# Kernel tuning notes

Measured on AMD Instinct MI355X. Metric: run time of the kernel, lower is better.

## Reference

```python
import jax, jax.numpy as jnp
import numpy as np

N_NODES = 50000
N_EDGES = 800000
C_IN = 128
HID = 128
C_OUT = 128


def _glorot(key, shape):
    fan_in, fan_out = shape
    lim = (6.0 / (fan_in + fan_out)) ** 0.5
    return jax.random.uniform(key, shape, jnp.float32, -lim, lim)


def setup_inputs() -> dict:
    key = jax.random.key(0)
    ks = jax.random.split(key, 8)
    x = jax.random.normal(ks[0], (N_NODES, C_IN), jnp.float32)
    edge_index = jax.random.randint(ks[1], (2, N_EDGES), 0, N_NODES, jnp.int32)
    return {
        "x": x,
        "edge_index": edge_index,
        # nn_in: Lin(2*C_IN, HID) -> ReLU -> Lin(HID, HID)
        "W1_in": _glorot(ks[2], (2 * C_IN, HID)), "b1_in": jnp.zeros((HID,), jnp.float32),
        "W2_in": _glorot(ks[3], (HID, HID)), "b2_in": jnp.zeros((HID,), jnp.float32),
        # nn_hid: Lin(2*HID, HID) -> ReLU -> Lin(HID, HID)
        "W1_hid": _glorot(ks[4], (2 * HID, HID)), "b1_hid": jnp.zeros((HID,), jnp.float32),
        "W2_hid": _glorot(ks[5], (HID, HID)), "b2_hid": jnp.zeros((HID,), jnp.float32),
        # nn_out: Lin(2*HID, HID) -> ReLU -> Lin(HID, C_OUT)
        "W1_out": _glorot(ks[6], (2 * HID, HID)), "b1_out": jnp.zeros((HID,), jnp.float32),
        "W2_out": _glorot(ks[7], (HID, C_OUT)), "b2_out": jnp.zeros((C_OUT,), jnp.float32),
    }


def _edge_conv(x, src, dst, W1, b1, W2, b2, n_nodes):
    # PyG EdgeConv: message = nn(concat(x_i, x_j - x_i)), aggr='max' over incoming edges
    xi = x[dst]                                   # [E, C] destination (center) nodes
    xj = x[src]                                   # [E, C] source (neighbor) nodes
    m = jnp.concatenate([xi, xj - xi], axis=-1)   # [E, 2C]
    h = jax.nn.relu(m @ W1 + b1) @ W2 + b2        # [E, H]
    agg = jax.ops.segment_max(h, dst, num_segments=n_nodes)  # [N, H]
    # PyG fills nodes with no incoming edges with 0 (segment_max yields -inf)
    return jnp.where(jnp.isfinite(agg), agg, 0.0)


def reference(x, edge_index, W1_in, b1_in, W2_in, b2_in,
              W1_hid, b1_hid, W2_hid, b2_hid,
              W1_out, b1_out, W2_out, b2_out):
    src, dst = edge_index[0], edge_index[1]
    n = x.shape[0]
    x = _edge_conv(x, src, dst, W1_in, b1_in, W2_in, b2_in, n)
    x = jax.nn.relu(x)
    x = _edge_conv(x, src, dst, W1_hid, b1_hid, W2_hid, b2_hid, n)
    x = jax.nn.relu(x)
    x = _edge_conv(x, src, dst, W1_out, b1_out, W2_out, b2_out, n)
    return x
```

## Files before the change

### kernel.cpp

```cpp
#include <hip/hip_runtime.h>

#define CH 128

typedef _Float16 f16;
typedef _Float16 f16x8 __attribute__((ext_vector_type(8)));
typedef float f32x4 __attribute__((ext_vector_type(4)));

__device__ __forceinline__ f32x4 mfma16(f16x8 a, f16x8 b, f32x4 c) {
    return __builtin_amdgcn_mfma_f32_16x16x32_f16(a, b, c, 0, 0, 0);
}

__global__ __launch_bounds__(256) void k_front(const int* __restrict__ edst, int* __restrict__ counts, int E,
                                               const float* __restrict__ W1a, const float* __restrict__ W2a,
                                               const float* __restrict__ W1b, const float* __restrict__ W2b,
                                               const float* __restrict__ W1c, const float* __restrict__ W2c,
                                               f16* __restrict__ WcT, f16* __restrict__ W2T,
                                               const float* __restrict__ x, f16* __restrict__ act,
                                               int total4, int gHist) {
    int bid = blockIdx.x;
    if (bid < gHist) {
        int e = bid * 256 + threadIdx.x;
        if (e < E) atomicAdd(&counts[edst[e]], 1);
    } else if (bid < gHist + 576) {
        int r = bid - gHist;
        int l = r / 192;
        const float* W1 = (l == 0) ? W1a : (l == 1) ? W1b : W1c;
        const float* W2 = (l == 0) ? W2a : (l == 1) ? W2b : W2c;
        f16* wct = WcT + l * 256 * CH;
        f16* w2t = W2T + l * CH * CH;
        int id = (r % 192) * 256 + threadIdx.x;
        if (id < 32768) {
            int n = id >> 7, k = id & 127;
            float v;
            if (n < CH) v = W1[k * CH + n] - W1[(CH + k) * CH + n];
            else        v = W1[(CH + k) * CH + (n - CH)];
            wct[n * CH + k] = (f16)v;
        } else {
            int rr = id - 32768;
            int n = rr >> 7, k = rr & 127;
            w2t[n * CH + k] = (f16)W2[k * CH + n];
        }
    } else {
        int i = (bid - gHist - 576) * 256 + threadIdx.x;
        if (i < total4) {
            float4 v = ((const float4*)x)[i];
            f16 h0 = (f16)v.x, h1 = (f16)v.y, h2 = (f16)v.z, h3 = (f16)v.w;
            short4 s;
            s.x = *(short*)&h0; s.y = *(short*)&h1; s.z = *(short*)&h2; s.w = *(short*)&h3;
            ((short4*)act)[i] = s;
        }
    }
}

__global__ __launch_bounds__(256) void k_scan1(const int* __restrict__ counts, int* __restrict__ row_ptr,
                                               int* __restrict__ blockSums, int n) {
    __shared__ int s[256];
    int t = threadIdx.x;
    int i = blockIdx.x * 256 + t;
    s[t] = (i < n) ? counts[i] : 0;
    __syncthreads();
    for (int off = 1; off < 256; off <<= 1) {
        int x = (t >= off) ? s[t - off] : 0;
        __syncthreads();
        s[t] += x;
        __syncthreads();
    }
    if (i < n) row_ptr[i + 1] = s[t];
    if (t == 255) blockSums[blockIdx.x] = s[255];
}

__global__ __launch_bounds__(256) void k_scan2(const int* __restrict__ blockSums, int* __restrict__ blockOff, int nb) {
    __shared__ int s[256];
    int t = threadIdx.x;
    s[t] = (t < nb) ? blockSums[t] : 0;
    __syncthreads();
    for (int off = 1; off < 256; off <<= 1) {
        int x = (t >= off) ? s[t - off] : 0;
        __syncthreads();
        s[t] += x;
        __syncthreads();
    }
    blockOff[t] = (t == 0) ? 0 : s[t - 1];
}

__global__ __launch_bounds__(256) void k_scan3(int* __restrict__ row_ptr, const int* __restrict__ blockOff, int n) {
    int i = blockIdx.x * 256 + threadIdx.x;
    if (i < n) row_ptr[i + 1] += blockOff[blockIdx.x];
    if (blockIdx.x == 0 && threadIdx.x == 0) row_ptr[0] = 0;
}

__global__ __launch_bounds__(256) void k_scatter(const int* __restrict__ src, const int* __restrict__ dst,
                                                 const int* __restrict__ row_ptr, int* __restrict__ cursor,
                                                 int* __restrict__ sed, int E) {
    int e = blockIdx.x * 256 + threadIdx.x;
    if (e < E) {
        int d = dst[e];
        int pos = row_ptr[d] + atomicAdd(&cursor[d], 1);
        sed[pos] = src[e];
    }
}

__global__ __launch_bounds__(256) void k_gemm1(const f16* __restrict__ act, const f16* __restrict__ WcT,
                                               const float* __restrict__ b1,
                                               f16* __restrict__ P, f16* __restrict__ Q, int nrows) {
    int t = threadIdx.x;
    int w = t >> 6, lane = t & 63;
    int m = lane & 15, q = lane >> 4;
    int rowbase = blockIdx.x * 256 + w * 64;
    f16x8 a[4][4];
#pragma unroll
    for (int rt = 0; rt < 4; ++rt) {
        int rowc = min(rowbase + rt * 16 + m, nrows - 1);
#pragma unroll
        for (int kk = 0; kk < 4; ++kk)
            a[rt][kk] = *(const f16x8*)(act + (size_t)rowc * CH + kk * 32 + q * 8);
    }
#pragma unroll
    for (int nb = 0; nb < 16; ++nb) {
        f16x8 b[4];
#pragma unroll
        for (int kk = 0; kk < 4; ++kk)
            b[kk] = *(const f16x8*)(WcT + (nb * 16 + m) * CH + kk * 32 + q * 8);
        int col = nb * 16 + m;
        float bias = (nb < 8) ? b1[col] : 0.f;
#pragma unroll
        for (int rt = 0; rt < 4; ++rt) {
            f32x4 acc = {0.f, 0.f, 0.f, 0.f};
#pragma unroll
            for (int kk = 0; kk < 4; ++kk) acc = mfma16(a[rt][kk], b[kk], acc);
#pragma unroll
            for (int r = 0; r < 4; ++r) {
                int ro = rowbase + rt * 16 + q * 4 + r;
                if (ro < nrows) {
                    float v = acc[r] + bias;
                    if (nb < 8) P[(size_t)ro * CH + col] = (f16)v;
                    else        Q[(size_t)ro * CH + (col - CH)] = (f16)v;
                }
            }
        }
    }
}

__global__ __launch_bounds__(256, 3)
void k_node(const f16* __restrict__ P, const f16* __restrict__ Q,
            const f16* __restrict__ W2Tg, const float* __restrict__ b2,
            const int* __restrict__ row_ptr, const int* __restrict__ sed,
            f16* __restrict__ act_out, float* __restrict__ final_out,
            int n_nodes, int flags, int nwv) {
    __shared__ __align__(16) f16 w2lds[8 * 4 * 64 * 8];

    int t = threadIdx.x;
    int w = t >> 6, lane = t & 63;
    int m = lane & 15, q = lane >> 4;

#pragma unroll
    for (int i = t; i < 2048; i += 256) {
        int nb = i >> 8, rem = i & 255, kk = rem >> 6, ln = rem & 63;
        int mm = ln & 15, qq = ln >> 4;
        *(f16x8*)&w2lds[i * 8] = *(const f16x8*)(W2Tg + (size_t)(nb * 16 + mm) * CH + kk * 32 + qq * 8);
    }
    __syncthreads();

    float biasA = b2[lane], biasB = b2[lane + 64];
    const f16x8 z8 = {};
    const f32x4 z4 = {0.f, 0.f, 0.f, 0.f};

    auto tile = [&](const f16x8* pf, const f16x8* qs, float* rmax) {
        unsigned wo = 0;
        asm volatile("" : "+v"(wo));
        const f16* wb = w2lds + wo + (size_t)lane * 8;
        f32x4 acc[8];
#pragma unroll
        for (int kk = 0; kk < 4; ++kk) {
            f16x8 af = __builtin_elementwise_max(pf[kk] + qs[kk], z8);
#pragma unroll
            for (int nb = 0; nb < 8; ++nb) {
                f16x8 bq = *(const f16x8*)(wb + (nb * 4 + kk) * 512);
                acc[nb] = (kk == 0) ? mfma16(af, bq, z4) : mfma16(af, bq, acc[nb]);
            }
        }
#pragma unroll
        for (int nb = 0; nb < 8; ++nb)
            rmax[nb] = fmaxf(fmaxf(fmaxf(acc[nb][0], acc[nb][1]),
                                   fmaxf(acc[nb][2], acc[nb][3])), rmax[nb]);
    };

    int nA = blockIdx.x * 4 + w;
    if (nA >= n_nodes) return;
    int nmax = n_nodes - 1;

    int rsA = row_ptr[nA], reA = row_ptr[nA + 1];
    int nB = nA + nwv; int nBc = min(nB, nmax);
    int rsB = row_ptr[nBc], reB = row_ptr[nBc + 1];
    int nC = nB + nwv; int nCc = min(nC, nmax);
    int rsC = row_ptr[nCc], reC = row_ptr[nCc + 1];

    int lA = (reA > rsA) ? reA - 1 : 0;
    int idx0A = sed[min(rsA + m, lA)];
    int idx1A = sed[min(rsA + 16 + m, lA)];
    int lB = (reB > rsB) ? reB - 1 : 0;
    int idx0B = sed[min(rsB + m, lB)];
    int idx1B = sed[min(rsB + 16 + m, lB)];

    f16x8 pfA[4], qs0A[4];
#pragma unroll
    for (int kk = 0; kk < 4; ++kk) {
        pfA[kk]  = *(const f16x8*)(P + (size_t)nA * CH + kk * 32 + q * 8);
        qs0A[kk] = *(const f16x8*)(Q + (size_t)idx0A * CH + kk * 32 + q * 8);
    }

    while (true) {
        f16x8 qs1A[4] = {};
        if (reA - rsA > 16) {
#pragma unroll
            for (int kk = 0; kk < 4; ++kk)
                qs1A[kk] = *(const f16x8*)(Q + (size_t)idx1A * CH + kk * 32 + q * 8);
        }
        f16x8 qs0B[4], pfB[4];
#pragma unroll
        for (int kk = 0; kk < 4; ++kk) {
            qs0B[kk] = *(const f16x8*)(Q + (size_t)idx0B * CH + kk * 32 + q * 8);
            pfB[kk]  = *(const f16x8*)(P + (size_t)nBc * CH + kk * 32 + q * 8);
        }
        int lC = (reC > rsC) ? reC - 1 : 0;
        int idx0C = sed[min(rsC + m, lC)];
        int idx1C = sed[min(rsC + 16 + m, lC)];
        int nD = nC + nwv; int nDc = min(nD, nmax);
        int rsD = row_ptr[nDc], reD = row_ptr[nDc + 1];

        float o0 = 0.f, o1 = 0.f;
        if (reA > rsA) {
            float rmax[8];
#pragma unroll
            for (int nb = 0; nb < 8; ++nb) rmax[nb] = -3.4e38f;
            tile(pfA, qs0A, rmax);
            if (reA - rsA > 16) tile(pfA, qs1A, rmax);
            for (int tb = rsA + 32; tb < reA; tb += 16) {
                int s2 = sed[min(tb + m, reA - 1)];
                f16x8 qx[4];
#pragma unroll
                for (int kk = 0; kk < 4; ++kk)
                    qx[kk] = *(const f16x8*)(Q + (size_t)s2 * CH + kk * 32 + q * 8);
                tile(pfA, qx, rmax);
            }
#pragma unroll
            for (int nb = 0; nb < 8; ++nb) {
                float v = rmax[nb];
                v = fmaxf(v, __shfl_xor(v, 16));
                v = fmaxf(v, __shfl_xor(v, 32));
                rmax[nb] = v;
            }
            float vA = (q & 2) ? ((q & 1) ? rmax[3] : rmax[2]) : ((q & 1) ? rmax[1] : rmax[0]);
            float vB = (q & 2) ? ((q & 1) ? rmax[7] : rmax[6]) : ((q & 1) ? rmax[5] : rmax[4]);
            o0 = vA + biasA;
            o1 = vB + biasB;
            if (flags & 1) { o0 = fmaxf(o0, 0.f); o1 = fmaxf(o1, 0.f); }
        }
        if (flags & 2) {
            float* orow = final_out + (size_t)nA * CH;
            orow[lane] = o0; orow[lane + 64] = o1;
        } else {
            f16* orow = act_out + (size_t)nA * CH;
            orow[lane] = (f16)o0; orow[lane + 64] = (f16)o1;
        }

        if (nB >= n_nodes) break;

        nA = nB; rsA = rsB; reA = reB; idx1A = idx1B;
#pragma unroll
        for (int kk = 0; kk < 4; ++kk) { qs0A[kk] = qs0B[kk]; pfA[kk] = pfB[kk]; }
        idx0B = idx0C; idx1B = idx1C;
        nB = nC; nBc = nCc; rsB = rsC; reB = reC;
        nC = nD; nCc = nDc; rsC = rsD; reC = reD;
    }
}

extern "C" void kernel_launch(void* const* d_in, const int* in_sizes, int n_in,
                              void* d_out, int out_size, void* d_ws, size_t ws_size,
                              hipStream_t stream) {
    const float* x = (const float*)d_in[0];
    const int* ei  = (const int*)d_in[1];
    int E = in_sizes[1] / 2;
    int N = in_sizes[0] / CH;
    const int* esrc = ei;
    const int* edst = ei + E;

    const float* W1[3] = {(const float*)d_in[2], (const float*)d_in[6],  (const float*)d_in[10]};
    const float* B1[3] = {(const float*)d_in[3], (const float*)d_in[7],  (const float*)d_in[11]};
    const float* W2[3] = {(const float*)d_in[4], (const float*)d_in[8],  (const float*)d_in[12]};
    const float* B2[3] = {(const float*)d_in[5], (const float*)d_in[9],  (const float*)d_in[13]};

    char* base = (char*)d_ws;
    size_t off = 0;
    auto alloc = [&](size_t bytes) -> void* {
        void* p = base + off;
        off = (off + bytes + 255) & ~(size_t)255;
        return p;
    };
    int* counts    = (int*)alloc(sizeof(int) * (size_t)(N + 256));
    int* cursor    = (int*)alloc(sizeof(int) * (size_t)(N + 256));
    size_t zero_bytes = off;
    int* row_ptr   = (int*)alloc(sizeof(int) * (size_t)(N + 1));
    int* blockSums = (int*)alloc(sizeof(int) * 256);
    int* blockOff  = (int*)alloc(sizeof(int) * 256);
    int* sed       = (int*)alloc(sizeof(int) * (size_t)E);
    f16* act       = (f16*)alloc(sizeof(f16) * (size_t)N * CH);
    f16* Pb        = (f16*)alloc(sizeof(f16) * (size_t)N * CH);
    f16* Qb        = (f16*)alloc(sizeof(f16) * (size_t)N * CH);
    f16* WcT       = (f16*)alloc(sizeof(f16) * 3 * 256 * CH);
    f16* W2T       = (f16*)alloc(sizeof(f16) * 3 * CH * CH);

    hipMemsetAsync(d_ws, 0, zero_bytes, stream);

    int gE = (E + 255) / 256;
    int gN = (N + 255) / 256;
    int total4 = N * CH / 4;
    int gCvt = (total4 + 255) / 256;
    k_front<<<gE + 576 + gCvt, 256, 0, stream>>>(edst, counts, E,
                                                 W1[0], W2[0], W1[1], W2[1], W1[2], W2[2],
                                                 WcT, W2T, x, act, total4, gE);
    k_scan1<<<gN, 256, 0, stream>>>(counts, row_ptr, blockSums, N);
    k_scan2<<<1, 256, 0, stream>>>(blockSums, blockOff, gN);
    k_scan3<<<gN, 256, 0, stream>>>(row_ptr, blockOff, N);
    k_scatter<<<gE, 256, 0, stream>>>(esrc, edst, row_ptr, cursor, sed, E);

    int gNode = 768;
    if (gNode > (N + 3) / 4) gNode = (N + 3) / 4;
    int nwv = gNode * 4;
    int gG1 = (N + 255) / 256;
    for (int l = 0; l < 3; ++l) {
        k_gemm1<<<gG1, 256, 0, stream>>>(act, WcT + l * 256 * CH, B1[l], Pb, Qb, N);
        int flags = (l < 2) ? 1 : 2;
        k_node<<<gNode, 256, 0, stream>>>(Pb, Qb, W2T + l * CH * CH, B2[l],
                                          row_ptr, sed, act, (float*)d_out, N, flags, nwv);
    }
}
```

Measured before the change: 450.0 us.

## Record edge ranks during histogram, prefetch second neighbor tile earlier, raise node occupancy

The histogram atomic's return value is stored as a per-edge rank, so the scatter pass no longer needs a second atomic on a cursor array, and the cursor memset goes away. In the node kernel, the second 16-neighbor gather for the next node is now issued one iteration earlier alongside the other prefetches, which hides more gather latency. Launch bounds go from 3 to 4 blocks per CU and the grid from 768 to 1024 blocks to raise occupancy. The risks are extra register pressure from the added prefetch buffers, which the tighter launch bound may turn into spills, plus an extra E-sized rank array to write and read.

After: 673.1 us. 49.6% more time.

```diff
diff --git a/kernel.cpp b/kernel.cpp
--- a/kernel.cpp
+++ b/kernel.cpp
@@ -10,7 +10,8 @@
     return __builtin_amdgcn_mfma_f32_16x16x32_f16(a, b, c, 0, 0, 0);
 }
 
-__global__ __launch_bounds__(256) void k_front(const int* __restrict__ edst, int* __restrict__ counts, int E,
+__global__ __launch_bounds__(256) void k_front(const int* __restrict__ edst, int* __restrict__ counts,
+                                               int* __restrict__ erank, int E,
                                                const float* __restrict__ W1a, const float* __restrict__ W2a,
                                                const float* __restrict__ W1b, const float* __restrict__ W2b,
                                                const float* __restrict__ W1c, const float* __restrict__ W2c,
@@ -20,7 +21,7 @@
     int bid = blockIdx.x;
     if (bid < gHist) {
         int e = bid * 256 + threadIdx.x;
-        if (e < E) atomicAdd(&counts[edst[e]], 1);
+        if (e < E) erank[e] = atomicAdd(&counts[edst[e]], 1);
     } else if (bid < gHist + 576) {
         int r = bid - gHist;
         int l = r / 192;
@@ -90,12 +91,11 @@
 }
 
 __global__ __launch_bounds__(256) void k_scatter(const int* __restrict__ src, const int* __restrict__ dst,
-                                                 const int* __restrict__ row_ptr, int* __restrict__ cursor,
+                                                 const int* __restrict__ row_ptr, const int* __restrict__ erank,
                                                  int* __restrict__ sed, int E) {
     int e = blockIdx.x * 256 + threadIdx.x;
     if (e < E) {
-        int d = dst[e];
-        int pos = row_ptr[d] + atomicAdd(&cursor[d], 1);
+        int pos = row_ptr[dst[e]] + erank[e];
         sed[pos] = src[e];
     }
 }
@@ -141,7 +141,7 @@
     }
 }
 
-__global__ __launch_bounds__(256, 3)
+__global__ __launch_bounds__(256, 4)
 void k_node(const f16* __restrict__ P, const f16* __restrict__ Q,
             const f16* __restrict__ W2Tg, const float* __restrict__ b2,
             const int* __restrict__ row_ptr, const int* __restrict__ sed,
@@ -202,25 +202,29 @@
     int idx0B = sed[min(rsB + m, lB)];
     int idx1B = sed[min(rsB + 16 + m, lB)];
 
-    f16x8 pfA[4], qs0A[4];
+    f16x8 pfA[4], qs0A[4], qs1A[4] = {};
 #pragma unroll
     for (int kk = 0; kk < 4; ++kk) {
         pfA[kk]  = *(const f16x8*)(P + (size_t)nA * CH + kk * 32 + q * 8);
         qs0A[kk] = *(const f16x8*)(Q + (size_t)idx0A * CH + kk * 32 + q * 8);
     }
+    if (reA - rsA > 16) {
+#pragma unroll
+        for (int kk = 0; kk < 4; ++kk)
+            qs1A[kk] = *(const f16x8*)(Q + (size_t)idx1A * CH + kk * 32 + q * 8);
+    }
 
     while (true) {
-        f16x8 qs1A[4] = {};
-        if (reA - rsA > 16) {
-#pragma unroll
-            for (int kk = 0; kk < 4; ++kk)
-                qs1A[kk] = *(const f16x8*)(Q + (size_t)idx1A * CH + kk * 32 + q * 8);
-        }
-        f16x8 qs0B[4], pfB[4];
+        f16x8 qs0B[4], pfB[4], qs1B[4] = {};
 #pragma unroll
         for (int kk = 0; kk < 4; ++kk) {
             qs0B[kk] = *(const f16x8*)(Q + (size_t)idx0B * CH + kk * 32 + q * 8);
             pfB[kk]  = *(const f16x8*)(P + (size_t)nBc * CH + kk * 32 + q * 8);
+        }
+        if (reB - rsB > 16) {
+#pragma unroll
+            for (int kk = 0; kk < 4; ++kk)
+                qs1B[kk] = *(const f16x8*)(Q + (size_t)idx1B * CH + kk * 32 + q * 8);
         }
         int lC = (reC > rsC) ? reC - 1 : 0;
         int idx0C = sed[min(rsC + m, lC)];
@@ -266,9 +270,9 @@
 
         if (nB >= n_nodes) break;
 
-        nA = nB; rsA = rsB; reA = reB; idx1A = idx1B;
-#pragma unroll
-        for (int kk = 0; kk < 4; ++kk) { qs0A[kk] = qs0B[kk]; pfA[kk] = pfB[kk]; }
+        nA = nB; rsA = rsB; reA = reB;
+#pragma unroll
+        for (int kk = 0; kk < 4; ++kk) { qs0A[kk] = qs0B[kk]; qs1A[kk] = qs1B[kk]; pfA[kk] = pfB[kk]; }
         idx0B = idx0C; idx1B = idx1C;
         nB = nC; nBc = nCc; rsB = rsC; reB = reC;
         nC = nD; nCc = nDc; rsC = rsD; reC = reD;
@@ -298,8 +302,8 @@
         return p;
     };
     int* counts    = (int*)alloc(sizeof(int) * (size_t)(N + 256));
-    int* cursor    = (int*)alloc(sizeof(int) * (size_t)(N + 256));
     size_t zero_bytes = off;
+    int* erank     = (int*)alloc(sizeof(int) * (size_t)E);
     int* row_ptr   = (int*)alloc(sizeof(int) * (size_t)(N + 1));
     int* blockSums = (int*)alloc(sizeof(int) * 256);
     int* blockOff  = (int*)alloc(sizeof(int) * 256);
@@ -316,15 +320,15 @@
     int gN = (N + 255) / 256;
     int total4 = N * CH / 4;
     int gCvt = (total4 + 255) / 256;
-    k_front<<<gE + 576 + gCvt, 256, 0, stream>>>(edst, counts, E,
+    k_front<<<gE + 576 + gCvt, 256, 0, stream>>>(edst, counts, erank, E,
                                                  W1[0], W2[0], W1[1], W2[1], W1[2], W2[2],
                                                  WcT, W2T, x, act, total4, gE);
     k_scan1<<<gN, 256, 0, stream>>>(counts, row_ptr, blockSums, N);
     k_scan2<<<1, 256, 0, stream>>>(blockSums, blockOff, gN);
     k_scan3<<<gN, 256, 0, stream>>>(row_ptr, blockOff, N);
-    k_scatter<<<gE, 256, 0, stream>>>(esrc, edst, row_ptr, cursor, sed, E);
-
-    int gNode = 768;
+    k_scatter<<<gE, 256, 0, stream>>>(esrc, edst, row_ptr, erank, sed, E);
+
+    int gNode = 1024;
     if (gNode > (N + 3) / 4) gNode = (N + 3) / 4;
     int nwv = gNode * 4;
     int gG1 = (N + 255) / 256;
```
